# Kernel tuning notes

Measured on AMD Instinct MI355X. Metric: run time of the kernel, lower is better.

Reference implementation:

```python
import jax, jax.numpy as jnp
import numpy as np

CLIP_LIMIT = 10.0
NTILES = 8        # OpenCV createCLAHE default tileGridSize=(8,8)
NBINS = 256

_M_RGB2XYZ = jnp.array([[0.412453, 0.357580, 0.180423],
                        [0.212671, 0.715160, 0.072169],
                        [0.019334, 0.119193, 0.950227]], dtype=jnp.float32)
_M_XYZ2RGB = jnp.array([[ 3.240479, -1.537150, -0.498535],
                        [-0.969256,  1.875992,  0.041556],
                        [ 0.055648, -0.204043,  1.057311]], dtype=jnp.float32)
_WP = jnp.array([0.950456, 1.0, 1.088754], dtype=jnp.float32)  # D65 white point (OpenCV)
_EPS = 0.008856


def rgb2lab(rgb):  # rgb: [H,W,3] in [0,1]
    xyz = jnp.einsum('hwc,dc->hwd', rgb, _M_RGB2XYZ) / _WP
    f = jnp.where(xyz > _EPS, jnp.cbrt(xyz), 7.787 * xyz + 16.0 / 116.0)
    fx, fy, fz = f[..., 0], f[..., 1], f[..., 2]
    L = 116.0 * fy - 16.0
    a = 500.0 * (fx - fy)
    b = 200.0 * (fy - fz)
    return L, a, b


def lab2rgb(L, a, b):
    fy = (L + 16.0) / 116.0
    fx = fy + a / 500.0
    fz = fy - b / 200.0
    f = jnp.stack([fx, fy, fz], axis=-1)
    xyz = jnp.where(f ** 3 > _EPS, f ** 3, (f - 16.0 / 116.0) / 7.787) * _WP
    rgb = jnp.einsum('hwd,cd->hwc', xyz, _M_XYZ2RGB)
    return jnp.clip(rgb, 0.0, 1.0)


def clahe_channel(L8, clip_limit):
    # L8: [H,W] int32 in [0,255]
    H, W = L8.shape
    th, tw = H // NTILES, W // NTILES
    area = float(th * tw)
    # per-tile histograms via one scatter-add
    rows = jnp.arange(H) // th            # [H] tile row id
    cols = jnp.arange(W) // tw            # [W] tile col id
    tid = rows[:, None] * NTILES + cols[None, :]          # [H,W]
    flat = (tid * NBINS + L8).ravel()
    hist = jnp.zeros(NTILES * NTILES * NBINS, jnp.float32).at[flat].add(1.0)
    hist = hist.reshape(NTILES * NTILES, NBINS)
    # clip + uniform redistribution of excess
    clip = max(clip_limit * area / NBINS, 1.0)
    excess = jnp.sum(jnp.maximum(hist - clip, 0.0), axis=1, keepdims=True)
    hist = jnp.minimum(hist, clip) + excess / NBINS
    # CDF -> LUT (OpenCV: lutScale = 255/tileArea, rounded)
    cdf = jnp.cumsum(hist, axis=1)
    lut = jnp.clip(jnp.round(cdf * (255.0 / area)), 0.0, 255.0)  # [T, 256]
    # bilinear interpolation between tile LUTs
    fy = jnp.clip((jnp.arange(H, dtype=jnp.float32) + 0.5) / th - 0.5, 0.0, NTILES - 1.0)
    fx = jnp.clip((jnp.arange(W, dtype=jnp.float32) + 0.5) / tw - 0.5, 0.0, NTILES - 1.0)
    y0 = jnp.floor(fy).astype(jnp.int32); y1 = jnp.minimum(y0 + 1, NTILES - 1)
    x0 = jnp.floor(fx).astype(jnp.int32); x1 = jnp.minimum(x0 + 1, NTILES - 1)
    wy = (fy - y0)[:, None]; wx = (fx - x0)[None, :]
    def g(yi, xi):  # gather LUT value for each pixel from tile (yi, xi)
        return lut[yi[:, None] * NTILES + xi[None, :], L8]
    top = (1.0 - wx) * g(y0, x0) + wx * g(y0, x1)
    bot = (1.0 - wx) * g(y1, x0) + wx * g(y1, x1)
    return (1.0 - wy) * top + wy * bot   # [H,W] float in [0,255]


def setup_inputs() -> dict:
    key = jax.random.key(0)
    x = jax.random.uniform(key, (3, 2048, 2048), dtype=jnp.float32)
    return {"x": x}


def reference(x) -> jnp.ndarray:
    hwc = jnp.transpose(x, (1, 2, 0))          # CHW -> HWC
    L, a, b = rgb2lab(hwc)                      # L in [0,100]
    L8 = jnp.clip(jnp.round(L * (255.0 / 100.0)), 0, 255).astype(jnp.int32)
    L_eq = clahe_channel(L8, CLIP_LIMIT) * (100.0 / 255.0)
    rgb = lab2rgb(L_eq, a, b)
    return jnp.transpose(rgb, (2, 0, 1))        # HWC -> CHW
```

## Files before the change

kernel.cpp:

```cpp
#include <hip/hip_runtime.h>
#include <stdint.h>

#define HW 4194304
#define WIDTH 2048
#define F(x) ((float)(x))

__device__ __forceinline__ float cbrtf_glibc(float x) {
    unsigned int bits = __float_as_uint(x);
    int xe = (int)((bits >> 23) & 0xFF) - 126;
    float xm = __uint_as_float((bits & 0x007FFFFFu) | 0x3F000000u);

    static const double factor[5] = {
        1.0 / 1.5874010519681994748,
        1.0 / 1.2599210498948731648,
        1.0,
        1.2599210498948731648,
        1.5874010519681994748
    };

    double xmd = (double)xm;
    double p = __dsub_rn(0.697570460207922770, __dmul_rn(0.191502161678719066, xmd));
    p = __dadd_rn(0.492659620528969547, __dmul_rn(p, xmd));
    float u = (float)p;

    float t2 = __fmul_rn(__fmul_rn(u, u), u);

    double ud  = (double)u;
    double t2d = (double)t2;
    double num = __dmul_rn(ud, __dadd_rn(t2d, __dmul_rn(2.0, xmd)));
    double den = __dadd_rn(__dmul_rn(2.0, t2d), xmd);
    double ym  = __dmul_rn(__ddiv_rn(num, den), factor[2 + (xe % 3)]);
    float ymf = (float)ym;

    return ldexpf(ymf, xe / 3);
}

__device__ __forceinline__ void rgb2lab_px(float r, float g, float b,
                                           int& l8, float& A_, float& B_) {
    float X = __fadd_rn(__fadd_rn(__fmul_rn(r, F(0.412453)), __fmul_rn(g, F(0.357580))), __fmul_rn(b, F(0.180423)));
    float Y = __fadd_rn(__fadd_rn(__fmul_rn(r, F(0.212671)), __fmul_rn(g, F(0.715160))), __fmul_rn(b, F(0.072169)));
    float Z = __fadd_rn(__fadd_rn(__fmul_rn(r, F(0.019334)), __fmul_rn(g, F(0.119193))), __fmul_rn(b, F(0.950227)));
    X = __fdiv_rn(X, F(0.950456));
    Z = __fdiv_rn(Z, F(1.088754));
    const float EPS = F(0.008856);
    const float C0  = F(16.0 / 116.0);
    float fx = (X > EPS) ? cbrtf_glibc(X) : __fadd_rn(__fmul_rn(F(7.787), X), C0);
    float fy = (Y > EPS) ? cbrtf_glibc(Y) : __fadd_rn(__fmul_rn(F(7.787), Y), C0);
    float fz = (Z > EPS) ? cbrtf_glibc(Z) : __fadd_rn(__fmul_rn(F(7.787), Z), C0);
    float L  = __fsub_rn(__fmul_rn(F(116.0), fy), F(16.0));
    A_ = __fmul_rn(F(500.0), __fsub_rn(fx, fy));
    B_ = __fmul_rn(F(200.0), __fsub_rn(fy, fz));
    float Lr = rintf(__fmul_rn(L, F(255.0 / 100.0)));
    Lr = fminf(fmaxf(Lr, 0.0f), 255.0f);
    l8 = (int)Lr;
}

__global__ __launch_bounds__(256) void k_hist(const float* __restrict__ x,
        unsigned int* __restrict__ hist,
        float* __restrict__ a_out, float* __restrict__ b_out,
        unsigned char* __restrict__ l8_out, int store) {
    __shared__ unsigned int h[2048];
    const int t = threadIdx.x;
    const int y = blockIdx.x;
    #pragma unroll
    for (int i = 0; i < 8; ++i) h[i * 256 + t] = 0;
    __syncthreads();
    const float* R  = x;
    const float* G  = x + HW;
    const float* Bp = x + 2 * HW;
    const int rowbase = y * WIDTH;
    #pragma unroll
    for (int c = 0; c < 8; ++c) {
        int col = c * 256 + t;
        int idx = rowbase + col;
        float r = R[idx], g = G[idx], b = Bp[idx];
        int l8; float A_, B_;
        rgb2lab_px(r, g, b, l8, A_, B_);
        if (store) {
            a_out[idx]  = A_;
            b_out[idx]  = B_;
            l8_out[idx] = (unsigned char)l8;
        }
        atomicAdd(&h[((col >> 8) << 8) + l8], 1u);
    }
    __syncthreads();
    const int tilerow = y >> 8;
    unsigned int* gh = hist + tilerow * 2048;
    #pragma unroll
    for (int i = 0; i < 8; ++i) {
        unsigned int v = h[i * 256 + t];
        if (v) atomicAdd(&gh[i * 256 + t], v);
    }
}

__global__ __launch_bounds__(256) void k_lut(const unsigned int* __restrict__ hist,
                                             float* __restrict__ lut) {
    __shared__ float sh[256];
    __shared__ float hc[256];
    const int t = threadIdx.x;
    const int tile = blockIdx.x;
    float h = (float)hist[tile * 256 + t];
    sh[t] = fmaxf(h - 2560.0f, 0.0f);
    __syncthreads();
    for (int s = 128; s > 0; s >>= 1) {
        if (t < s) sh[t] += sh[t + s];
        __syncthreads();
    }
    float excess = sh[0];
    hc[t] = __fadd_rn(fminf(h, 2560.0f), __fmul_rn(excess, F(1.0 / 256.0)));
    __syncthreads();
    if (t == 0) {
        float c = 0.0f;
        for (int i = 0; i < 256; ++i) { c = __fadd_rn(c, hc[i]); hc[i] = c; }
    }
    __syncthreads();
    float v = rintf(__fmul_rn(hc[t], F(255.0 / 65536.0)));
    lut[tile * 256 + t] = fminf(fmaxf(v, 0.0f), 255.0f);
}

__global__ __launch_bounds__(256) void k_apply(const float* __restrict__ x,
        const float* __restrict__ lut,
        const float* __restrict__ a_in, const float* __restrict__ b_in,
        const unsigned char* __restrict__ l8_in,
        float* __restrict__ out, int stored) {
    const int idx = blockIdx.x * 256 + threadIdx.x;
    const int y  = idx >> 11;
    const int xc = idx & 2047;
    int l8; float A_, B_;
    if (stored) {
        l8 = (int)l8_in[idx];
        A_ = a_in[idx];
        B_ = b_in[idx];
    } else {
        float r = x[idx], g = x[idx + HW], b = x[idx + 2 * HW];
        rgb2lab_px(r, g, b, l8, A_, B_);
    }
    float fyc = fminf(fmaxf(((float)y  + 0.5f) * (1.0f / 256.0f) - 0.5f, 0.0f), 7.0f);
    float fxc = fminf(fmaxf(((float)xc + 0.5f) * (1.0f / 256.0f) - 0.5f, 0.0f), 7.0f);
    int y0 = (int)floorf(fyc); int y1 = min(y0 + 1, 7);
    int x0 = (int)floorf(fxc); int x1 = min(x0 + 1, 7);
    float wy = fyc - (float)y0;
    float wx = fxc - (float)x0;
    float g00 = lut[(y0 * 8 + x0) * 256 + l8];
    float g01 = lut[(y0 * 8 + x1) * 256 + l8];
    float g10 = lut[(y1 * 8 + x0) * 256 + l8];
    float g11 = lut[(y1 * 8 + x1) * 256 + l8];
    float top = __fadd_rn(__fmul_rn(__fsub_rn(1.0f, wx), g00), __fmul_rn(wx, g01));
    float bot = __fadd_rn(__fmul_rn(__fsub_rn(1.0f, wx), g10), __fmul_rn(wx, g11));
    float Leq = __fmul_rn(__fadd_rn(__fmul_rn(__fsub_rn(1.0f, wy), top), __fmul_rn(wy, bot)),
                          F(100.0 / 255.0));
    const float EPS = F(0.008856);
    const float C0  = F(16.0 / 116.0);
    float fy2 = __fdiv_rn(__fadd_rn(Leq, 16.0f), 116.0f);
    float fx2 = __fadd_rn(fy2, __fdiv_rn(A_, 500.0f));
    float fz2 = __fsub_rn(fy2, __fdiv_rn(B_, 200.0f));
    float t3;
    t3 = fx2 * fx2 * fx2;
    float X = ((t3 > EPS) ? t3 : __fdiv_rn(__fsub_rn(fx2, C0), F(7.787))) * F(0.950456);
    t3 = fy2 * fy2 * fy2;
    float Y = ((t3 > EPS) ? t3 : __fdiv_rn(__fsub_rn(fy2, C0), F(7.787))) * F(1.0);
    t3 = fz2 * fz2 * fz2;
    float Z = ((t3 > EPS) ? t3 : __fdiv_rn(__fsub_rn(fz2, C0), F(7.787))) * F(1.088754);
    float rr = __fadd_rn(__fadd_rn(__fmul_rn(X, F(3.240479)),  __fmul_rn(Y, F(-1.537150))), __fmul_rn(Z, F(-0.498535)));
    float gg = __fadd_rn(__fadd_rn(__fmul_rn(X, F(-0.969256)), __fmul_rn(Y, F(1.875992))),  __fmul_rn(Z, F(0.041556)));
    float bb = __fadd_rn(__fadd_rn(__fmul_rn(X, F(0.055648)),  __fmul_rn(Y, F(-0.204043))), __fmul_rn(Z, F(1.057311)));
    rr = fminf(fmaxf(rr, 0.0f), 1.0f);
    gg = fminf(fmaxf(gg, 0.0f), 1.0f);
    bb = fminf(fmaxf(bb, 0.0f), 1.0f);
    out[idx]          = rr;
    out[idx + HW]     = gg;
    out[idx + 2 * HW] = bb;
}

extern "C" void kernel_launch(void* const* d_in, const int* in_sizes, int n_in,
                              void* d_out, int out_size, void* d_ws, size_t ws_size,
                              hipStream_t stream) {
    const float* x = (const float*)d_in[0];
    float* out = (float*)d_out;
    char* ws = (char*)d_ws;
    unsigned int* hist = (unsigned int*)ws;
    float* lut = (float*)(ws + 65536);
    const size_t off = 131072;
    float* a_buf = (float*)(ws + off);
    float* b_buf = (float*)(ws + off + (size_t)HW * 4);
    unsigned char* l8_buf = (unsigned char*)(ws + off + (size_t)HW * 8);
    const size_t need = off + (size_t)HW * 9;
    const int store = (ws_size >= need) ? 1 : 0;

    hipMemsetAsync(hist, 0, 65536, stream);
    k_hist<<<2048, 256, 0, stream>>>(x, hist, a_buf, b_buf, l8_buf, store);
    k_lut<<<64, 256, 0, stream>>>(hist, lut);
    k_apply<<<HW / 256, 256, 0, stream>>>(x, lut, a_buf, b_buf, l8_buf, out, store);
}
```

Baseline: 138.5 us.

## Interleave a/b intermediates as float2 and stage row LUTs in shared memory

The separate a and b intermediate buffers are merged into one interleaved float2 buffer, so each pixel's pair is written and read with a single 8-byte access. The apply kernel now runs one block per image row with 8 pixels per thread. Each block first copies the two tile-row LUT bands it needs (4096 floats) into shared memory, then does the bilinear LUT gathers from LDS instead of global memory. This trades fewer, larger blocks and a 16KB LDS footprint per block for cheaper gathers and fewer memory transactions.

```diff
diff --git a/kernel.cpp b/kernel.cpp
--- a/kernel.cpp
+++ b/kernel.cpp
@@ -57,7 +57,7 @@
 
 __global__ __launch_bounds__(256) void k_hist(const float* __restrict__ x,
         unsigned int* __restrict__ hist,
-        float* __restrict__ a_out, float* __restrict__ b_out,
+        float2* __restrict__ ab_out,
         unsigned char* __restrict__ l8_out, int store) {
     __shared__ unsigned int h[2048];
     const int t = threadIdx.x;
@@ -77,8 +77,7 @@
         int l8; float A_, B_;
         rgb2lab_px(r, g, b, l8, A_, B_);
         if (store) {
-            a_out[idx]  = A_;
-            b_out[idx]  = B_;
+            ab_out[idx] = make_float2(A_, B_);
             l8_out[idx] = (unsigned char)l8;
         }
         atomicAdd(&h[((col >> 8) << 8) + l8], 1u);
@@ -120,56 +119,75 @@
 
 __global__ __launch_bounds__(256) void k_apply(const float* __restrict__ x,
         const float* __restrict__ lut,
-        const float* __restrict__ a_in, const float* __restrict__ b_in,
+        const float2* __restrict__ ab_in,
         const unsigned char* __restrict__ l8_in,
         float* __restrict__ out, int stored) {
-    const int idx = blockIdx.x * 256 + threadIdx.x;
-    const int y  = idx >> 11;
-    const int xc = idx & 2047;
-    int l8; float A_, B_;
-    if (stored) {
-        l8 = (int)l8_in[idx];
-        A_ = a_in[idx];
-        B_ = b_in[idx];
-    } else {
-        float r = x[idx], g = x[idx + HW], b = x[idx + 2 * HW];
-        rgb2lab_px(r, g, b, l8, A_, B_);
-    }
-    float fyc = fminf(fmaxf(((float)y  + 0.5f) * (1.0f / 256.0f) - 0.5f, 0.0f), 7.0f);
-    float fxc = fminf(fmaxf(((float)xc + 0.5f) * (1.0f / 256.0f) - 0.5f, 0.0f), 7.0f);
+    __shared__ float lutS[4096];
+    const int t = threadIdx.x;
+    const int y = blockIdx.x;
+
+    float fyc = fminf(fmaxf(((float)y + 0.5f) * (1.0f / 256.0f) - 0.5f, 0.0f), 7.0f);
     int y0 = (int)floorf(fyc); int y1 = min(y0 + 1, 7);
-    int x0 = (int)floorf(fxc); int x1 = min(x0 + 1, 7);
-    float wy = fyc - (float)y0;
-    float wx = fxc - (float)x0;
-    float g00 = lut[(y0 * 8 + x0) * 256 + l8];
-    float g01 = lut[(y0 * 8 + x1) * 256 + l8];
-    float g10 = lut[(y1 * 8 + x0) * 256 + l8];
-    float g11 = lut[(y1 * 8 + x1) * 256 + l8];
-    float top = __fadd_rn(__fmul_rn(__fsub_rn(1.0f, wx), g00), __fmul_rn(wx, g01));
-    float bot = __fadd_rn(__fmul_rn(__fsub_rn(1.0f, wx), g10), __fmul_rn(wx, g11));
-    float Leq = __fmul_rn(__fadd_rn(__fmul_rn(__fsub_rn(1.0f, wy), top), __fmul_rn(wy, bot)),
-                          F(100.0 / 255.0));
-    const float EPS = F(0.008856);
-    const float C0  = F(16.0 / 116.0);
-    float fy2 = __fdiv_rn(__fadd_rn(Leq, 16.0f), 116.0f);
-    float fx2 = __fadd_rn(fy2, __fdiv_rn(A_, 500.0f));
-    float fz2 = __fsub_rn(fy2, __fdiv_rn(B_, 200.0f));
-    float t3;
-    t3 = fx2 * fx2 * fx2;
-    float X = ((t3 > EPS) ? t3 : __fdiv_rn(__fsub_rn(fx2, C0), F(7.787))) * F(0.950456);
-    t3 = fy2 * fy2 * fy2;
-    float Y = ((t3 > EPS) ? t3 : __fdiv_rn(__fsub_rn(fy2, C0), F(7.787))) * F(1.0);
-    t3 = fz2 * fz2 * fz2;
-    float Z = ((t3 > EPS) ? t3 : __fdiv_rn(__fsub_rn(fz2, C0), F(7.787))) * F(1.088754);
-    float rr = __fadd_rn(__fadd_rn(__fmul_rn(X, F(3.240479)),  __fmul_rn(Y, F(-1.537150))), __fmul_rn(Z, F(-0.498535)));
-    float gg = __fadd_rn(__fadd_rn(__fmul_rn(X, F(-0.969256)), __fmul_rn(Y, F(1.875992))),  __fmul_rn(Z, F(0.041556)));
-    float bb = __fadd_rn(__fadd_rn(__fmul_rn(X, F(0.055648)),  __fmul_rn(Y, F(-0.204043))), __fmul_rn(Z, F(1.057311)));
-    rr = fminf(fmaxf(rr, 0.0f), 1.0f);
-    gg = fminf(fmaxf(gg, 0.0f), 1.0f);
-    bb = fminf(fmaxf(bb, 0.0f), 1.0f);
-    out[idx]          = rr;
-    out[idx + HW]     = gg;
-    out[idx + 2 * HW] = bb;
+    float wy = __fsub_rn(fyc, (float)y0);
+    float omwy = __fsub_rn(1.0f, wy);
+
+    const float* ltop = lut + y0 * 2048;
+    const float* lbot = lut + y1 * 2048;
+    #pragma unroll
+    for (int i = 0; i < 8; ++i) {
+        lutS[i * 256 + t]        = ltop[i * 256 + t];
+        lutS[2048 + i * 256 + t] = lbot[i * 256 + t];
+    }
+    __syncthreads();
+
+    const int rowbase = y * WIDTH;
+    #pragma unroll
+    for (int c = 0; c < 8; ++c) {
+        int col = c * 256 + t;
+        int idx = rowbase + col;
+        int l8; float A_, B_;
+        if (stored) {
+            float2 ab = ab_in[idx];
+            A_ = ab.x; B_ = ab.y;
+            l8 = (int)l8_in[idx];
+        } else {
+            float r = x[idx], g = x[idx + HW], b = x[idx + 2 * HW];
+            rgb2lab_px(r, g, b, l8, A_, B_);
+        }
+        float fxc = fminf(fmaxf(((float)col + 0.5f) * (1.0f / 256.0f) - 0.5f, 0.0f), 7.0f);
+        int x0 = (int)floorf(fxc); int x1 = min(x0 + 1, 7);
+        float wx = __fsub_rn(fxc, (float)x0);
+        float omwx = __fsub_rn(1.0f, wx);
+        float g00 = lutS[x0 * 256 + l8];
+        float g01 = lutS[x1 * 256 + l8];
+        float g10 = lutS[2048 + x0 * 256 + l8];
+        float g11 = lutS[2048 + x1 * 256 + l8];
+        float top = __fadd_rn(__fmul_rn(omwx, g00), __fmul_rn(wx, g01));
+        float bot = __fadd_rn(__fmul_rn(omwx, g10), __fmul_rn(wx, g11));
+        float Leq = __fmul_rn(__fadd_rn(__fmul_rn(omwy, top), __fmul_rn(wy, bot)),
+                              F(100.0 / 255.0));
+        const float EPS = F(0.008856);
+        const float C0  = F(16.0 / 116.0);
+        float fy2 = __fdiv_rn(__fadd_rn(Leq, 16.0f), 116.0f);
+        float fx2 = __fadd_rn(fy2, __fdiv_rn(A_, 500.0f));
+        float fz2 = __fsub_rn(fy2, __fdiv_rn(B_, 200.0f));
+        float t3;
+        t3 = fx2 * fx2 * fx2;
+        float X = ((t3 > EPS) ? t3 : __fdiv_rn(__fsub_rn(fx2, C0), F(7.787))) * F(0.950456);
+        t3 = fy2 * fy2 * fy2;
+        float Y = ((t3 > EPS) ? t3 : __fdiv_rn(__fsub_rn(fy2, C0), F(7.787))) * F(1.0);
+        t3 = fz2 * fz2 * fz2;
+        float Z = ((t3 > EPS) ? t3 : __fdiv_rn(__fsub_rn(fz2, C0), F(7.787))) * F(1.088754);
+        float rr = __fadd_rn(__fadd_rn(__fmul_rn(X, F(3.240479)),  __fmul_rn(Y, F(-1.537150))), __fmul_rn(Z, F(-0.498535)));
+        float gg = __fadd_rn(__fadd_rn(__fmul_rn(X, F(-0.969256)), __fmul_rn(Y, F(1.875992))),  __fmul_rn(Z, F(0.041556)));
+        float bb = __fadd_rn(__fadd_rn(__fmul_rn(X, F(0.055648)),  __fmul_rn(Y, F(-0.204043))), __fmul_rn(Z, F(1.057311)));
+        rr = fminf(fmaxf(rr, 0.0f), 1.0f);
+        gg = fminf(fmaxf(gg, 0.0f), 1.0f);
+        bb = fminf(fmaxf(bb, 0.0f), 1.0f);
+        out[idx]          = rr;
+        out[idx + HW]     = gg;
+        out[idx + 2 * HW] = bb;
+    }
 }
 
 extern "C" void kernel_launch(void* const* d_in, const int* in_sizes, int n_in,
@@ -181,14 +199,13 @@
     unsigned int* hist = (unsigned int*)ws;
     float* lut = (float*)(ws + 65536);
     const size_t off = 131072;
-    float* a_buf = (float*)(ws + off);
-    float* b_buf = (float*)(ws + off + (size_t)HW * 4);
+    float2* ab_buf = (float2*)(ws + off);
     unsigned char* l8_buf = (unsigned char*)(ws + off + (size_t)HW * 8);
     const size_t need = off + (size_t)HW * 9;
     const int store = (ws_size >= need) ? 1 : 0;
 
-    hipMemsetAsync(hist, 0, 65536, stream);
-    k_hist<<<2048, 256, 0, stream>>>(x, hist, a_buf, b_buf, l8_buf, store);
+    (void)hipMemsetAsync(hist, 0, 65536, stream);
+    k_hist<<<2048, 256, 0, stream>>>(x, hist, ab_buf, l8_buf, store);
     k_lut<<<64, 256, 0, stream>>>(hist, lut);
-    k_apply<<<HW / 256, 256, 0, stream>>>(x, lut, a_buf, b_buf, l8_buf, out, store);
-}
+    k_apply<<<2048, 256, 0, stream>>>(x, lut, ab_buf, l8_buf, out, store);
+}
```

Result: faster. 135.5 us (-2.2%).
